# Kernel tuning notes

Measured on AMD Instinct MI355X. Metric: run time of the kernel, lower is better.

Reference implementation:

```python
import math
import jax, jax.numpy as jnp
import numpy as np

B, N, F_IN, F_H, F_OUT = 8, 2048, 128, 256, 256
RATIOS = (0.8, 0.5)
EDGE_P = 0.01  # adjacency density -> avg degree ~20


def setup_inputs() -> dict:
    key = jax.random.key(0)
    kx, ka, k1, k2, k3, k4, k5, k6 = jax.random.split(key, 8)
    x = jax.random.normal(kx, (B, N, F_IN), dtype=jnp.float32)
    u = jax.random.uniform(ka, (B, N, N), dtype=jnp.float32)
    # sparse nonneg weighted adjacency, zero diagonal (so gcn self-loop add == A + I)
    A = jnp.where(u < EDGE_P, u / EDGE_P, 0.0) * (1.0 - jnp.eye(N, dtype=jnp.float32))
    s_in, s_h = 1.0 / math.sqrt(F_IN), 1.0 / math.sqrt(F_H)
    W1 = jax.random.normal(k1, (F_IN, F_H), dtype=jnp.float32) * s_in
    b1 = jnp.zeros((F_H,), dtype=jnp.float32)
    p1 = jax.random.normal(k2, (F_H,), dtype=jnp.float32) * s_h
    W2 = jax.random.normal(k3, (F_H, F_OUT), dtype=jnp.float32) * s_h
    b2 = jnp.zeros((F_OUT,), dtype=jnp.float32)
    p2 = jax.random.normal(k4, (F_OUT,), dtype=jnp.float32) * s_h
    return {"x": x, "A": A, "W1": W1, "b1": b1, "p1": p1, "W2": W2, "b2": b2, "p2": p2}


def _gcn(x, A, W, b):
    # PyG GCNConv with gcn_norm: A_hat = A + I (diag(A)==0), deg = in-degree (col sums),
    # out[i] = sum_j dinv[j] * A_hat[j, i] * dinv[i] * (xW)[j] + b
    n = A.shape[0]
    A_hat = A + jnp.eye(n, dtype=A.dtype)
    dinv = jax.lax.rsqrt(A_hat.sum(axis=0))  # deg >= 1 due to self loops
    M = dinv[:, None] * A_hat * dinv[None, :]
    return M.T @ (x @ W) + b


def _topk_pool(x, A, p, k):
    # score = tanh(x @ p / ||p||); keep top-k nodes, scale features by score
    score = jnp.tanh((x @ p) / jnp.linalg.norm(p))
    vals, perm = jax.lax.top_k(score, k)
    return x[perm] * vals[:, None], A[perm][:, perm]


def _per_graph(x0, A0, W1, b1, p1, W2, b2, p2):
    n = x0.shape[0]
    k1 = math.ceil(RATIOS[0] * n)
    k2 = math.ceil(RATIOS[1] * k1)
    h = jax.nn.relu(_gcn(x0, A0, W1, b1))          # dropout is identity in eval mode
    h, A1 = _topk_pool(h, A0, p1, k1)
    h = jax.nn.relu(_gcn(h, A1, W2, b2))
    h, _ = _topk_pool(h, A1, p2, k2)
    # node_mask in the source is always all-True, so mean-fill never triggers:
    # rows [:k2] = pooled features, rest zeros.
    return jnp.zeros((n, h.shape[1]), dtype=h.dtype).at[:k2].set(h)


def reference(x, A, W1, b1, p1, W2, b2, p2):
    f = lambda xi, Ai: _per_graph(xi, Ai, W1, b1, p1, W2, b2, p2)
    return jax.vmap(f)(x, A)  # [B, N, F_OUT]
```

## Files before the change

kernel.cpp:

```cpp
#include <hip/hip_runtime.h>
#include <math.h>

#define BATCH 8
#define NN    2048
#define FIN   128
#define FH    256
#define KP1   1639
#define KP2   820
#define CAP   64

__global__ __launch_bounds__(256) void init_all(int* __restrict__ cnt,
                                                int* __restrict__ inv,
                                                const float* __restrict__ p1,
                                                const float* __restrict__ p2,
                                                double* __restrict__ norms) {
  int t = blockIdx.x * 256 + threadIdx.x;
  if (t < BATCH * NN) { cnt[t] = 0; inv[t] = -1; }
  if (blockIdx.x == 0) {
    __shared__ double red[256];
    int f = threadIdx.x;
    double v = (double)p1[f];
    red[f] = v * v;
    __syncthreads();
    for (int s = 128; s > 0; s >>= 1) { if (f < s) red[f] += red[f + s]; __syncthreads(); }
    if (f == 0) norms[0] = sqrt(red[0]);
    __syncthreads();
    v = (double)p2[f];
    red[f] = v * v;
    __syncthreads();
    for (int s = 128; s > 0; s >>= 1) { if (f < s) red[f] += red[f + s]; __syncthreads(); }
    if (f == 0) norms[1] = sqrt(red[0]);
  }
}

__global__ void build_csc1(const float* __restrict__ A, int* __restrict__ cnt,
                           int* __restrict__ idx, float* __restrict__ val) {
  const int total = BATCH * NN * (NN / 4);
  for (int t = blockIdx.x * blockDim.x + threadIdx.x; t < total;
       t += gridDim.x * blockDim.x) {
    float4 v4 = reinterpret_cast<const float4*>(A)[t];
    int b = t / (NN * NN / 4);
    int rem = t % (NN * NN / 4);
    int j = rem / (NN / 4);
    int i0 = (rem % (NN / 4)) * 4;
    float vv[4] = {v4.x, v4.y, v4.z, v4.w};
#pragma unroll
    for (int c = 0; c < 4; ++c) {
      float v = vv[c];
      if (v != 0.0f) {
        int col = b * NN + i0 + c;
        int p = atomicAdd(&cnt[col], 1);
        if (p < CAP) { idx[col * CAP + p] = j; val[col * CAP + p] = v; }
      }
    }
  }
}

__global__ __launch_bounds__(256) void canon_cols(int* __restrict__ cnt,
                                                  int* __restrict__ idx,
                                                  float* __restrict__ val,
                                                  double* __restrict__ dinv) {
  int wid = (blockIdx.x * blockDim.x + threadIdx.x) >> 6;
  int lane = threadIdx.x & 63;
  if (wid >= BATCH * NN) return;
  int c = cnt[wid]; if (c > CAP) c = CAP;
  if (lane == 0) cnt[wid] = c;
  int key = 0x7fffffff;
  float v = 0.0f;
  if (lane < c) {
    key = idx[(size_t)wid * CAP + lane];
    v = val[(size_t)wid * CAP + lane];
  }
#pragma unroll
  for (int k = 2; k <= 64; k <<= 1) {
#pragma unroll
    for (int j = k >> 1; j > 0; j >>= 1) {
      int pk = __shfl_xor(key, j);
      float pv = __shfl_xor(v, j);
      bool up = ((lane & k) == 0);
      bool takeMin = (((lane & j) == 0) == up);
      bool sw = takeMin ? (pk < key) : (pk > key);
      if (sw) { key = pk; v = pv; }
    }
  }
  if (lane < c) {
    idx[(size_t)wid * CAP + lane] = key;
    val[(size_t)wid * CAP + lane] = v;
  }
  double dv = (double)v;
#pragma unroll
  for (int off = 32; off > 0; off >>= 1) dv += __shfl_xor(dv, off);
  if (lane == 0) dinv[wid] = 1.0 / sqrt(1.0 + dv);
}

template <int KD, typename TX>
__global__ __launch_bounds__(512) void gemm_y(const TX* __restrict__ X,
                                              const float* __restrict__ W,
                                              const double* __restrict__ dinv,
                                              double* __restrict__ Y, int rows) {
  const int KC = 32;
  int b = blockIdx.y;
  int r0 = blockIdx.x * 32;
  int t = threadIdx.x;
  int fq = (t & 63) * 4;
  int rg = (t >> 6) * 4;
  __shared__ TX xs[32][KC];
  __shared__ float wsh[KC][FH];
  const TX* Xb = X + (size_t)b * NN * KD;
  double acc[4][4];
#pragma unroll
  for (int r = 0; r < 4; ++r)
#pragma unroll
    for (int c = 0; c < 4; ++c) acc[r][c] = 0.0;

  for (int kc = 0; kc < KD; kc += KC) {
    __syncthreads();
    for (int e = t; e < 32 * KC; e += 512) {
      int r = e >> 5, k = e & 31;
      int row = r0 + r;
      xs[r][k] = (row < rows) ? Xb[(size_t)row * KD + kc + k] : (TX)0;
    }
    for (int e = t; e < KC * FH / 4; e += 512) {
      int k = e >> 6;
      int f = (e << 2) & 255;
      *reinterpret_cast<float4*>(&wsh[k][f]) =
          *reinterpret_cast<const float4*>(&W[(size_t)(kc + k) * FH + f]);
    }
    __syncthreads();
#pragma unroll 2
    for (int k = 0; k < KC; k += 2) {
      float4 waf = *reinterpret_cast<const float4*>(&wsh[k][fq]);
      float4 wbf = *reinterpret_cast<const float4*>(&wsh[k + 1][fq]);
      double wa0 = (double)waf.x, wa1 = (double)waf.y;
      double wa2 = (double)waf.z, wa3 = (double)waf.w;
      double wb0 = (double)wbf.x, wb1 = (double)wbf.y;
      double wb2 = (double)wbf.z, wb3 = (double)wbf.w;
#pragma unroll
      for (int r = 0; r < 4; ++r) {
        double x0 = (double)xs[rg + r][k];
        double x1 = (double)xs[rg + r][k + 1];
        acc[r][0] = fma(x1, wb0, fma(x0, wa0, acc[r][0]));
        acc[r][1] = fma(x1, wb1, fma(x0, wa1, acc[r][1]));
        acc[r][2] = fma(x1, wb2, fma(x0, wa2, acc[r][2]));
        acc[r][3] = fma(x1, wb3, fma(x0, wa3, acc[r][3]));
      }
    }
  }
#pragma unroll
  for (int r = 0; r < 4; ++r) {
    int row = r0 + rg + r;
    if (row < rows) {
      double d = dinv[b * NN + row];
      double* o = Y + ((size_t)b * NN + row) * FH + fq;
      o[0] = d * acc[r][0];
      o[1] = d * acc[r][1];
      o[2] = d * acc[r][2];
      o[3] = d * acc[r][3];
    }
  }
}

__global__ __launch_bounds__(FH) void aggregate(
    const double* __restrict__ Y, const int* __restrict__ cnt,
    const int* __restrict__ idx, const float* __restrict__ val,
    const double* __restrict__ dinv, const float* __restrict__ bias,
    const float* __restrict__ p, double* __restrict__ H, double* __restrict__ dot) {
  int b = blockIdx.x & 7, i = blockIdx.x >> 3, f = threadIdx.x;
  int col = b * NN + i;
  const int* ji = idx + (size_t)col * CAP;
  const float* jv = val + (size_t)col * CAP;
  const double* Yb = Y + (size_t)b * NN * FH;
  double acc = Y[(size_t)col * FH + f];
  int c = cnt[col];
  int a = 0;
  for (; a + 8 <= c; a += 8) {
    double tt[8];
    double vv[8];
#pragma unroll
    for (int u = 0; u < 8; ++u) {
      vv[u] = (double)jv[a + u];
      tt[u] = Yb[(size_t)ji[a + u] * FH + f];
    }
#pragma unroll
    for (int u = 0; u < 8; ++u) acc += vv[u] * tt[u];
  }
  for (; a < c; ++a) {
    acc += (double)jv[a] * Yb[(size_t)ji[a] * FH + f];
  }
  double h = fmax(dinv[col] * acc + (double)bias[f], 0.0);
  H[(size_t)col * FH + f] = h;
  double pd = h * (double)p[f];
#pragma unroll
  for (int off = 32; off > 0; off >>= 1) pd += __shfl_xor(pd, off);
  __shared__ double red[4];
  if ((f & 63) == 0) red[f >> 6] = pd;
  __syncthreads();
  if (f == 0) dot[col] = (red[0] + red[1]) + (red[2] + red[3]);
}

__global__ __launch_bounds__(1024) void topk_sort(
    const double* __restrict__ dot, const double* __restrict__ norms, int which,
    int valid, int k, int* __restrict__ perm, double* __restrict__ vals) {
  __shared__ double sk[NN];
  __shared__ int si[NN];
  int b = blockIdx.x, t = threadIdx.x;
  double nrm = norms[which];
  for (int e = t; e < NN; e += 1024) {
    sk[e] = (e < valid) ? tanh(dot[b * NN + e] / nrm) : -1.0e300;
    si[e] = e;
  }
  for (int kk = 2; kk <= NN; kk <<= 1) {
    for (int j = kk >> 1; j > 0; j >>= 1) {
      __syncthreads();
      int i = ((t & ~(j - 1)) << 1) | (t & (j - 1));
      int q = i | j;
      double ka = sk[i], kb = sk[q];
      int ia = si[i], ib = si[q];
      bool p_first = (kb > ka) || (kb == ka && ib < ia);
      bool up = ((i & kk) == 0);
      if (up ? p_first : !p_first) { sk[i] = kb; sk[q] = ka; si[i] = ib; si[q] = ia; }
    }
  }
  __syncthreads();
  for (int e = t; e < k; e += 1024) {
    perm[b * NN + e] = si[e];
    vals[b * NN + e] = sk[e];
  }
}

__global__ __launch_bounds__(FH) void pool1_kernel(
    const double* __restrict__ H, const int* __restrict__ perm,
    const double* __restrict__ vals, double* __restrict__ HP, int* __restrict__ inv) {
  int b = blockIdx.x & 7, r = blockIdx.x >> 3, f = threadIdx.x;
  int node = perm[b * NN + r];
  double s = vals[b * NN + r];
  if (f == 0) inv[b * NN + node] = r;
  HP[((size_t)b * NN + r) * FH + f] = H[((size_t)b * NN + node) * FH + f] * s;
}

__global__ __launch_bounds__(256) void build_csc2(
    const int* __restrict__ cnt1, const int* __restrict__ idx1,
    const float* __restrict__ val1, const int* __restrict__ perm,
    const int* __restrict__ inv, int* __restrict__ cnt2, int* __restrict__ idx2,
    float* __restrict__ val2, double* __restrict__ dinv2) {
  int wid = (blockIdx.x * blockDim.x + threadIdx.x) >> 6;
  int lane = threadIdx.x & 63;
  if (wid >= BATCH * KP1) return;
  int b = wid / KP1, ri = wid % KP1;
  int colA = b * NN + perm[b * NN + ri];
  int c = cnt1[colA];
  int rj = -1;
  float v = 0.0f;
  if (lane < c) {
    int j = idx1[(size_t)colA * CAP + lane];
    v = val1[(size_t)colA * CAP + lane];
    rj = inv[b * NN + j];
  }
  bool keep = (lane < c) && (rj >= 0);
  unsigned long long mask = __ballot(keep);
  int pos = __popcll(mask & ((1ull << lane) - 1ull));
  int colB = b * NN + ri;
  if (keep) {
    idx2[(size_t)colB * CAP + pos] = rj;
    val2[(size_t)colB * CAP + pos] = v;
  }
  if (lane == 0) cnt2[colB] = (int)__popcll(mask);
  double dv = keep ? (double)v : 0.0;
#pragma unroll
  for (int off = 32; off > 0; off >>= 1) dv += __shfl_xor(dv, off);
  if (lane == 0) dinv2[colB] = 1.0 / sqrt(1.0 + dv);
}

__global__ __launch_bounds__(FH) void final_kernel(
    const double* __restrict__ H2, const int* __restrict__ perm2,
    const double* __restrict__ vals2, float* __restrict__ out) {
  int b = blockIdx.x & 7, r = blockIdx.x >> 3, f = threadIdx.x;
  float o = 0.0f;
  if (r < KP2) {
    int rr = perm2[b * NN + r];
    o = (float)(H2[((size_t)b * NN + rr) * FH + f] * vals2[b * NN + r]);
  }
  out[((size_t)b * NN + r) * FH + f] = o;
}

extern "C" void kernel_launch(void* const* d_in, const int* in_sizes, int n_in,
                              void* d_out, int out_size, void* d_ws, size_t ws_size,
                              hipStream_t stream) {
  const float* x  = (const float*)d_in[0];
  const float* A  = (const float*)d_in[1];
  const float* W1 = (const float*)d_in[2];
  const float* b1 = (const float*)d_in[3];
  const float* p1 = (const float*)d_in[4];
  const float* W2 = (const float*)d_in[5];
  const float* b2 = (const float*)d_in[6];
  const float* p2 = (const float*)d_in[7];
  float* out = (float*)d_out;

  char* ws = (char*)d_ws;
  size_t off = 0;
  auto alloc = [&](size_t bytes) {
    void* p = ws + off;
    off += (bytes + 255) & ~(size_t)255;
    return p;
  };
  double* dot   = (double*)alloc((size_t)BATCH * NN * 8);
  double* y     = (double*)alloc((size_t)BATCH * NN * FH * 8);
  double* h     = (double*)alloc((size_t)BATCH * NN * FH * 8);
  double* hp    = (double*)alloc((size_t)BATCH * NN * FH * 8);
  double* dinv1 = (double*)alloc((size_t)BATCH * NN * 8);
  double* dinv2 = (double*)alloc((size_t)BATCH * NN * 8);
  int*   cnt1  = (int*)alloc((size_t)BATCH * NN * 4);
  int*   idx1  = (int*)alloc((size_t)BATCH * NN * CAP * 4);
  float* val1  = (float*)alloc((size_t)BATCH * NN * CAP * 4);
  int*   cnt2  = (int*)alloc((size_t)BATCH * NN * 4);
  int*   idx2  = (int*)alloc((size_t)BATCH * NN * CAP * 4);
  float* val2  = (float*)alloc((size_t)BATCH * NN * CAP * 4);
  int*   perm1 = (int*)alloc((size_t)BATCH * NN * 4);
  double* vals1 = (double*)alloc((size_t)BATCH * NN * 8);
  int*   perm2 = (int*)alloc((size_t)BATCH * NN * 4);
  double* vals2 = (double*)alloc((size_t)BATCH * NN * 8);
  int*   inv   = (int*)alloc((size_t)BATCH * NN * 4);
  double* norms = (double*)alloc(64);

  init_all<<<BATCH * NN / 256, 256, 0, stream>>>(cnt1, inv, p1, p2, norms);
  build_csc1<<<4096, 256, 0, stream>>>(A, cnt1, idx1, val1);
  canon_cols<<<(BATCH * NN * 64) / 256, 256, 0, stream>>>(cnt1, idx1, val1, dinv1);
  gemm_y<FIN, float><<<dim3(NN / 32, BATCH), 512, 0, stream>>>(x, W1, dinv1, y, NN);
  aggregate<<<NN * BATCH, FH, 0, stream>>>(y, cnt1, idx1, val1, dinv1, b1, p1, h, dot);
  topk_sort<<<BATCH, 1024, 0, stream>>>(dot, norms, 0, NN, KP1, perm1, vals1);
  pool1_kernel<<<KP1 * BATCH, FH, 0, stream>>>(h, perm1, vals1, hp, inv);
  build_csc2<<<(BATCH * KP1 * 64 + 255) / 256, 256, 0, stream>>>(cnt1, idx1, val1, perm1,
                                                                 inv, cnt2, idx2, val2, dinv2);
  gemm_y<FH, double><<<dim3((KP1 + 31) / 32, BATCH), 512, 0, stream>>>(hp, W2, dinv2, y, KP1);
  aggregate<<<KP1 * BATCH, FH, 0, stream>>>(y, cnt2, idx2, val2, dinv2, b2, p2, h, dot);
  topk_sort<<<BATCH, 1024, 0, stream>>>(dot, norms, 1, KP1, KP2, perm2, vals2);
  final_kernel<<<NN * BATCH, FH, 0, stream>>>(h, perm2, vals2, out);
}
```

Measured before the change: 313.3 us.

## Fuse top-k pooling gather into second GEMM and drop pool kernel

Removes the separate pool1 kernel, which copied selected rows of H scaled by their scores into an intermediate buffer. That gather and scaling now happen while loading X tiles inside gemm_y, and topk_sort writes the inverse permutation directly. The GEMM grid is also flattened so consecutive blocks cycle through batches. This drops a large double-precision intermediate write and read and one launch, at the cost of indirect, less coalesced row loads inside the GEMM.

```diff
diff --git a/kernel.cpp b/kernel.cpp
--- a/kernel.cpp
+++ b/kernel.cpp
@@ -93,14 +93,17 @@
   if (lane == 0) dinv[wid] = 1.0 / sqrt(1.0 + dv);
 }
 
-template <int KD, typename TX>
+template <int KD, typename TX, bool GATHER>
 __global__ __launch_bounds__(512) void gemm_y(const TX* __restrict__ X,
                                               const float* __restrict__ W,
                                               const double* __restrict__ dinv,
-                                              double* __restrict__ Y, int rows) {
+                                              double* __restrict__ Y, int rows,
+                                              const int* __restrict__ perm,
+                                              const double* __restrict__ gvals) {
   const int KC = 32;
-  int b = blockIdx.y;
-  int r0 = blockIdx.x * 32;
+  int bid = blockIdx.x;
+  int b = bid & 7;
+  int r0 = (bid >> 3) * 32;
   int t = threadIdx.x;
   int fq = (t & 63) * 4;
   int rg = (t >> 6) * 4;
@@ -118,7 +121,17 @@
     for (int e = t; e < 32 * KC; e += 512) {
       int r = e >> 5, k = e & 31;
       int row = r0 + r;
-      xs[r][k] = (row < rows) ? Xb[(size_t)row * KD + kc + k] : (TX)0;
+      if (GATHER) {
+        if (row < rows) {
+          int src = perm[b * NN + row];
+          double scl = gvals[b * NN + row];
+          xs[r][k] = (TX)(X[((size_t)b * NN + src) * KD + kc + k] * scl);
+        } else {
+          xs[r][k] = (TX)0;
+        }
+      } else {
+        xs[r][k] = (row < rows) ? Xb[(size_t)row * KD + kc + k] : (TX)0;
+      }
     }
     for (int e = t; e < KC * FH / 4; e += 512) {
       int k = e >> 6;
@@ -200,7 +213,8 @@
 
 __global__ __launch_bounds__(1024) void topk_sort(
     const double* __restrict__ dot, const double* __restrict__ norms, int which,
-    int valid, int k, int* __restrict__ perm, double* __restrict__ vals) {
+    int valid, int k, int* __restrict__ perm, double* __restrict__ vals,
+    int* __restrict__ inv) {
   __shared__ double sk[NN];
   __shared__ int si[NN];
   int b = blockIdx.x, t = threadIdx.x;
@@ -223,19 +237,11 @@
   }
   __syncthreads();
   for (int e = t; e < k; e += 1024) {
-    perm[b * NN + e] = si[e];
+    int node = si[e];
+    perm[b * NN + e] = node;
     vals[b * NN + e] = sk[e];
-  }
-}
-
-__global__ __launch_bounds__(FH) void pool1_kernel(
-    const double* __restrict__ H, const int* __restrict__ perm,
-    const double* __restrict__ vals, double* __restrict__ HP, int* __restrict__ inv) {
-  int b = blockIdx.x & 7, r = blockIdx.x >> 3, f = threadIdx.x;
-  int node = perm[b * NN + r];
-  double s = vals[b * NN + r];
-  if (f == 0) inv[b * NN + node] = r;
-  HP[((size_t)b * NN + r) * FH + f] = H[((size_t)b * NN + node) * FH + f] * s;
+    inv[b * NN + node] = e;
+  }
 }
 
 __global__ __launch_bounds__(256) void build_csc2(
@@ -306,7 +312,6 @@
   double* dot   = (double*)alloc((size_t)BATCH * NN * 8);
   double* y     = (double*)alloc((size_t)BATCH * NN * FH * 8);
   double* h     = (double*)alloc((size_t)BATCH * NN * FH * 8);
-  double* hp    = (double*)alloc((size_t)BATCH * NN * FH * 8);
   double* dinv1 = (double*)alloc((size_t)BATCH * NN * 8);
   double* dinv2 = (double*)alloc((size_t)BATCH * NN * 8);
   int*   cnt1  = (int*)alloc((size_t)BATCH * NN * 4);
@@ -325,14 +330,15 @@
   init_all<<<BATCH * NN / 256, 256, 0, stream>>>(cnt1, inv, p1, p2, norms);
   build_csc1<<<4096, 256, 0, stream>>>(A, cnt1, idx1, val1);
   canon_cols<<<(BATCH * NN * 64) / 256, 256, 0, stream>>>(cnt1, idx1, val1, dinv1);
-  gemm_y<FIN, float><<<dim3(NN / 32, BATCH), 512, 0, stream>>>(x, W1, dinv1, y, NN);
+  gemm_y<FIN, float, false><<<(NN / 32) * BATCH, 512, 0, stream>>>(
+      x, W1, dinv1, y, NN, nullptr, nullptr);
   aggregate<<<NN * BATCH, FH, 0, stream>>>(y, cnt1, idx1, val1, dinv1, b1, p1, h, dot);
-  topk_sort<<<BATCH, 1024, 0, stream>>>(dot, norms, 0, NN, KP1, perm1, vals1);
-  pool1_kernel<<<KP1 * BATCH, FH, 0, stream>>>(h, perm1, vals1, hp, inv);
+  topk_sort<<<BATCH, 1024, 0, stream>>>(dot, norms, 0, NN, KP1, perm1, vals1, inv);
   build_csc2<<<(BATCH * KP1 * 64 + 255) / 256, 256, 0, stream>>>(cnt1, idx1, val1, perm1,
                                                                  inv, cnt2, idx2, val2, dinv2);
-  gemm_y<FH, double><<<dim3((KP1 + 31) / 32, BATCH), 512, 0, stream>>>(hp, W2, dinv2, y, KP1);
+  gemm_y<FH, double, true><<<((KP1 + 31) / 32) * BATCH, 512, 0, stream>>>(
+      h, W2, dinv2, y, KP1, perm1, vals1);
   aggregate<<<KP1 * BATCH, FH, 0, stream>>>(y, cnt2, idx2, val2, dinv2, b2, p2, h, dot);
-  topk_sort<<<BATCH, 1024, 0, stream>>>(dot, norms, 1, KP1, KP2, perm2, vals2);
+  topk_sort<<<BATCH, 1024, 0, stream>>>(dot, norms, 1, KP1, KP2, perm2, vals2, inv);
   final_kernel<<<NN * BATCH, FH, 0, stream>>>(h, perm2, vals2, out);
 }
```

Result: faster. 298.9 us (-4.6%).
